# Optimization experiments

Measured on AMD Instinct MI355X. Metric: run time of the kernel, lower is better.

Reference implementation:

```python
import jax, jax.numpy as jnp
import numpy as np

NUM_RBF = 300
RADIUS_RES = 0.1
GAMMA = 10.0
HIDDEN = 64
MB, ATOM = 32, 64


def setup_inputs() -> dict:
    key = jax.random.key(0)
    ks = jax.random.split(key, 12)
    def lin(kw, kb, fan_in, fan_out):
        lim = 1.0 / np.sqrt(fan_in)
        W = jax.random.uniform(kw, (fan_out, fan_in), jnp.float32, -lim, lim)
        b = jax.random.uniform(kb, (fan_out,), jnp.float32, -lim, lim)
        return W, b
    W1, b1 = lin(ks[0], ks[1], HIDDEN, HIDDEN)
    W2, b2 = lin(ks[2], ks[3], HIDDEN, HIDDEN)
    W3, b3 = lin(ks[4], ks[5], HIDDEN, HIDDEN)
    Wd1, bd1 = lin(ks[6], ks[7], NUM_RBF, HIDDEN)
    Wd2, bd2 = lin(ks[8], ks[9], HIDDEN, HIDDEN)
    x = jax.random.normal(ks[10], (MB, ATOM, HIDDEN), jnp.float32)
    dist = jax.random.uniform(ks[11], (MB, ATOM, ATOM), jnp.float32, 0.0, 10.0)
    return {"x": x, "dist": dist,
            "W1": W1, "b1": b1, "W2": W2, "b2": b2, "W3": W3, "b3": b3,
            "Wd1": Wd1, "bd1": bd1, "Wd2": Wd2, "bd2": bd2}


def reference(x, dist, W1, b1, W2, b2, W3, b3, Wd1, bd1, Wd2, bd2):
    sp = jax.nn.softplus
    # linear1 applied per-atom
    v = jnp.einsum('mic,oc->mio', x, W1) + b1                      # [mb, atom, h]
    # CFConv: gaussian RBF expansion of pairwise distances
    centers = jnp.arange(NUM_RBF, dtype=jnp.float32) * RADIUS_RES  # [rbf]
    rbf = jnp.exp(-GAMMA * (dist[..., None] - centers) ** 2)       # [mb, a, a, rbf]
    # 2-layer filter MLP on each pair
    f = sp(jnp.einsum('mijr,hr->mijh', rbf, Wd1) + bd1)            # [mb, a, a, h]
    f = sp(jnp.einsum('mijh,oh->mijo', f, Wd2) + bd2)              # [mb, a, a, h]
    # broadcast-multiply v over pairs and reduce over source atom i (dim=1)
    v = jnp.einsum('mic,mijc->mjc', v, f)                          # [mb, atom, h]
    v = sp(jnp.einsum('mic,oc->mio', v, W2) + b2)
    v = jnp.einsum('mic,oc->mio', v, W3) + b3
    return x + v
```

## Files before the change

kernel.cpp:

```cpp
#include <hip/hip_runtime.h>
#include <math.h>

#define MB_    32
#define ATOM_  64
#define HID_   64
#define NRBF_  300
#define GAMMA_ 10.0f
#define RES_   0.1f

#define TPTS      2001
#define TSTEP     0.005f
#define INV_TSTEP 200.0f

#define RWIN 28

#define T_OFF   0
#define T_SZ    (TPTS * 64)
#define V1_OFF  (T_OFF + T_SZ)
#define V1_SZ   (MB_ * 64 * 64)
#define W2T_OFF (V1_OFF + V1_SZ)
#define W3T_OFF (W2T_OFF + 4096)

__device__ __forceinline__ float sp_f(float x) {
    return fmaxf(x, 0.f) + log1pf(__expf(-fabsf(x)));
}

__global__ __launch_bounds__(256)
void schnet_prep(const float* __restrict__ x,   const float* __restrict__ W1,
                 const float* __restrict__ b1,  const float* __restrict__ W2,
                 const float* __restrict__ W3,  const float* __restrict__ Wd1,
                 const float* __restrict__ bd1, const float* __restrict__ Wd2,
                 const float* __restrict__ bd2, float* __restrict__ ws)
{
    __shared__ float smem[8320];
    const int tid = threadIdx.x;
    const int b   = blockIdx.x;

    if (b < MB_) {
        float* sx = smem;
        float* sw = smem + 4160;
        const float* xm = x + b * 4096;
        for (int e = tid; e < 4096; e += 256) {
            int i = e >> 6, c = e & 63;
            sx[i * 65 + c] = xm[e];
            sw[i * 65 + c] = W1[e];
        }
        __syncthreads();
        const int tx = tid & 15;
        const int ty = tid >> 4;
        float acc[4][4];
        #pragma unroll
        for (int aa = 0; aa < 4; ++aa)
            #pragma unroll
            for (int bb = 0; bb < 4; ++bb)
                acc[aa][bb] = b1[4 * tx + bb];
        #pragma unroll 8
        for (int k = 0; k < 64; ++k) {
            float xa[4], wb[4];
            #pragma unroll
            for (int aa = 0; aa < 4; ++aa) xa[aa] = sx[(4 * ty + aa) * 65 + k];
            #pragma unroll
            for (int bb = 0; bb < 4; ++bb) wb[bb] = sw[(4 * tx + bb) * 65 + k];
            #pragma unroll
            for (int aa = 0; aa < 4; ++aa)
                #pragma unroll
                for (int bb = 0; bb < 4; ++bb)
                    acc[aa][bb] = fmaf(xa[aa], wb[bb], acc[aa][bb]);
        }
        #pragma unroll
        for (int aa = 0; aa < 4; ++aa) {
            float4 v = make_float4(acc[aa][0], acc[aa][1], acc[aa][2], acc[aa][3]);
            *(float4*)(ws + V1_OFF + (b * 64 + 4 * ty + aa) * 64 + 4 * tx) = v;
        }
    } else if (b < MB_ + 501) {
        float* su = smem;
        const int sub = tid >> 6, c = tid & 63;
        const int s  = (b - MB_) * 4 + sub;
        const int se = min(s, TPTS - 1);
        const float d = se * TSTEP;

        int r0 = (int)ceilf((d - 1.35f) * 10.0f);
        r0 = max(r0, 0);

        float a0 = bd1[c], a1 = 0.f;
        const float* wrow1 = Wd1 + c * NRBF_ + r0;
        #pragma unroll
        for (int k = 0; k < RWIN; k += 2) {
            float t0 = fmaf(-RES_, (float)(r0 + k),     d);
            float t1 = fmaf(-RES_, (float)(r0 + k + 1), d);
            float w0 = __expf(-GAMMA_ * t0 * t0);
            float w1 = __expf(-GAMMA_ * t1 * t1);
            a0 = fmaf(w0, wrow1[k],     a0);
            a1 = fmaf(w1, wrow1[k + 1], a1);
        }
        su[sub * 64 + c] = sp_f(a0 + a1);
        __syncthreads();

        const float4* wrow2 = (const float4*)(Wd2 + c * 64);
        const float*  uu    = su + sub * 64;
        float s0 = bd2[c], s1 = 0.f, s2 = 0.f, s3 = 0.f;
        #pragma unroll
        for (int h4 = 0; h4 < 16; ++h4) {
            float4 wv = wrow2[h4];
            s0 = fmaf(wv.x, uu[4 * h4 + 0], s0);
            s1 = fmaf(wv.y, uu[4 * h4 + 1], s1);
            s2 = fmaf(wv.z, uu[4 * h4 + 2], s2);
            s3 = fmaf(wv.w, uu[4 * h4 + 3], s3);
        }
        if (s < TPTS)
            ws[T_OFF + s * 64 + c] = sp_f((s0 + s1) + (s2 + s3));
    } else {
        for (int e = tid; e < 4096; e += 256) {
            int o = e >> 6, c = e & 63;
            ws[W2T_OFF + c * 64 + o] = W2[e];
            ws[W3T_OFF + c * 64 + o] = W3[e];
        }
    }
}

__global__ __launch_bounds__(256)
void schnet_main(const float* __restrict__ x, const float* __restrict__ dist,
                 const float* __restrict__ b2, const float* __restrict__ b3,
                 const float* __restrict__ ws, float* __restrict__ out)
{
    __shared__ float sD[64];
    __shared__ float sRed[4 * 64];
    const int m   = blockIdx.x >> 6;
    const int j   = blockIdx.x & 63;
    const int tid = threadIdx.x;
    const int c   = tid & 63;
    const int p   = tid >> 6;

    if (tid < 64) sD[tid] = dist[(m * ATOM_ + tid) * ATOM_ + j];
    __syncthreads();

    const float* Tb  = ws + T_OFF;
    const float* v1m = ws + V1_OFF + (m * 64 + p * 16) * 64;
    float acc = 0.f;
    #pragma unroll
    for (int ii = 0; ii < 16; ++ii) {
        float d  = sD[p * 16 + ii];
        float f  = d * INV_TSTEP;
        int   s  = min((int)f, TPTS - 2);
        float fr = f - (float)s;
        const float* Tr = Tb + s * 64;
        float t0 = Tr[c], t1 = Tr[64 + c];
        float f2v = fmaf(fr, t1 - t0, t0);
        acc = fmaf(f2v, v1m[ii * 64 + c], acc);
    }
    sRed[p * 64 + c] = acc;
    __syncthreads();
    if (tid < 64)
        sD[tid] = sRed[tid] + sRed[64 + tid] + sRed[128 + tid] + sRed[192 + tid];
    __syncthreads();

    {
        const float* W2t = ws + W2T_OFF;
        float s_ = 0.f;
        #pragma unroll
        for (int cc = 0; cc < 16; ++cc)
            s_ = fmaf(sD[16 * p + cc], W2t[(16 * p + cc) * 64 + c], s_);
        sRed[p * 64 + c] = s_;
    }
    __syncthreads();
    if (tid < 64)
        sD[tid] = sp_f(sRed[tid] + sRed[64 + tid] + sRed[128 + tid] + sRed[192 + tid] + b2[tid]);
    __syncthreads();
    {
        const float* W3t = ws + W3T_OFF;
        float s_ = 0.f;
        #pragma unroll
        for (int cc = 0; cc < 16; ++cc)
            s_ = fmaf(sD[16 * p + cc], W3t[(16 * p + cc) * 64 + c], s_);
        sRed[p * 64 + c] = s_;
    }
    __syncthreads();
    if (tid < 64) {
        float v_ = sRed[tid] + sRed[64 + tid] + sRed[128 + tid] + sRed[192 + tid] + b3[tid];
        out[(m * ATOM_ + j) * HID_ + tid] = v_ + x[(m * ATOM_ + j) * HID_ + tid];
    }
}

extern "C" void kernel_launch(void* const* d_in, const int* in_sizes, int n_in,
                              void* d_out, int out_size, void* d_ws, size_t ws_size,
                              hipStream_t stream) {
    const float* x   = (const float*)d_in[0];
    const float* dist= (const float*)d_in[1];
    const float* W1  = (const float*)d_in[2];
    const float* b1  = (const float*)d_in[3];
    const float* W2  = (const float*)d_in[4];
    const float* b2  = (const float*)d_in[5];
    const float* W3  = (const float*)d_in[6];
    const float* b3  = (const float*)d_in[7];
    const float* Wd1 = (const float*)d_in[8];
    const float* bd1 = (const float*)d_in[9];
    const float* Wd2 = (const float*)d_in[10];
    const float* bd2 = (const float*)d_in[11];
    float* out = (float*)d_out;
    float* ws  = (float*)d_ws;
    (void)in_sizes; (void)n_in; (void)out_size; (void)ws_size;

    schnet_prep<<<dim3(MB_ + 501 + 1), dim3(256), 0, stream>>>(
        x, W1, b1, W2, W3, Wd1, bd1, Wd2, bd2, ws);
    schnet_main<<<dim3(MB_ * ATOM_), dim3(256), 0, stream>>>(
        x, dist, b2, b3, ws, out);
}
```

Baseline: 92.88 us.

## Interleave lookup table pairs for float2 loads and stage filter weights in LDS

The filter lookup table now stores each sample's value next to the next sample's value, so the main kernel fetches both interpolation endpoints with a single float2 load instead of two scattered loads. This doubles the table's size and write traffic. In the prep kernel, each table-building block stages its Wd1 window and a transposed Wd2 in shared memory, replacing strided per-thread global reads with coalesced loads. The cost is extra shared memory use and an added barrier per block.

```diff
diff --git a/kernel.cpp b/kernel.cpp
--- a/kernel.cpp
+++ b/kernel.cpp
@@ -13,10 +13,11 @@
 #define INV_TSTEP 200.0f
 
 #define RWIN 28
-
-#define T_OFF   0
-#define T_SZ    (TPTS * 64)
-#define V1_OFF  (T_OFF + T_SZ)
+#define NSTG 32
+
+#define T2_OFF  0
+#define T2_SZ   (TPTS * 128)
+#define V1_OFF  (T2_OFF + T2_SZ)
 #define V1_SZ   (MB_ * 64 * 64)
 #define W2T_OFF (V1_OFF + V1_SZ)
 #define W3T_OFF (W2T_OFF + 4096)
@@ -41,9 +42,9 @@
         float* sw = smem + 4160;
         const float* xm = x + b * 4096;
         for (int e = tid; e < 4096; e += 256) {
-            int i = e >> 6, c = e & 63;
-            sx[i * 65 + c] = xm[e];
-            sw[i * 65 + c] = W1[e];
+            int i = e >> 6, cc = e & 63;
+            sx[i * 65 + cc] = xm[e];
+            sw[i * 65 + cc] = W1[e];
         }
         __syncthreads();
         const int tx = tid & 15;
@@ -73,47 +74,68 @@
             *(float4*)(ws + V1_OFF + (b * 64 + 4 * ty + aa) * 64 + 4 * tx) = v;
         }
     } else if (b < MB_ + 501) {
-        float* su = smem;
+        float* sWd1  = smem;
+        float* sWd2T = smem + NSTG * 65;
+        float* su    = smem + NSTG * 65 + 4160;
+
         const int sub = tid >> 6, c = tid & 63;
         const int s  = (b - MB_) * 4 + sub;
         const int se = min(s, TPTS - 1);
         const float d = se * TSTEP;
 
+        const int s0 = (b - MB_) * 4;
+        int rb0 = (int)ceilf((s0 * TSTEP - 1.35f) * 10.0f);
+        rb0 = max(rb0, 0);
         int r0 = (int)ceilf((d - 1.35f) * 10.0f);
         r0 = max(r0, 0);
 
+        #pragma unroll
+        for (int it = 0; it < (NSTG * 64) / 256; ++it) {
+            int idx = tid + it * 256;
+            int k   = idx & (NSTG - 1);
+            int cc  = idx >> 5;
+            sWd1[k * 65 + cc] = Wd1[cc * NRBF_ + rb0 + k];
+        }
+        #pragma unroll
+        for (int it = 0; it < 4096 / 256; ++it) {
+            int idx = tid + it * 256;
+            int h = idx & 63, o = idx >> 6;
+            sWd2T[h * 65 + o] = Wd2[idx];
+        }
+        __syncthreads();
+
         float a0 = bd1[c], a1 = 0.f;
-        const float* wrow1 = Wd1 + c * NRBF_ + r0;
+        const float* wr = sWd1 + (r0 - rb0) * 65 + c;
         #pragma unroll
         for (int k = 0; k < RWIN; k += 2) {
             float t0 = fmaf(-RES_, (float)(r0 + k),     d);
             float t1 = fmaf(-RES_, (float)(r0 + k + 1), d);
             float w0 = __expf(-GAMMA_ * t0 * t0);
             float w1 = __expf(-GAMMA_ * t1 * t1);
-            a0 = fmaf(w0, wrow1[k],     a0);
-            a1 = fmaf(w1, wrow1[k + 1], a1);
+            a0 = fmaf(w0, wr[k * 65],       a0);
+            a1 = fmaf(w1, wr[(k + 1) * 65], a1);
         }
         su[sub * 64 + c] = sp_f(a0 + a1);
         __syncthreads();
 
-        const float4* wrow2 = (const float4*)(Wd2 + c * 64);
-        const float*  uu    = su + sub * 64;
-        float s0 = bd2[c], s1 = 0.f, s2 = 0.f, s3 = 0.f;
-        #pragma unroll
-        for (int h4 = 0; h4 < 16; ++h4) {
-            float4 wv = wrow2[h4];
-            s0 = fmaf(wv.x, uu[4 * h4 + 0], s0);
-            s1 = fmaf(wv.y, uu[4 * h4 + 1], s1);
-            s2 = fmaf(wv.z, uu[4 * h4 + 2], s2);
-            s3 = fmaf(wv.w, uu[4 * h4 + 3], s3);
-        }
-        if (s < TPTS)
-            ws[T_OFF + s * 64 + c] = sp_f((s0 + s1) + (s2 + s3));
+        const float* uu = su + sub * 64;
+        float p0 = bd2[c], p1 = 0.f;
+        #pragma unroll
+        for (int h = 0; h < 64; h += 2) {
+            p0 = fmaf(sWd2T[h * 65 + c],       uu[h],     p0);
+            p1 = fmaf(sWd2T[(h + 1) * 65 + c], uu[h + 1], p1);
+        }
+        if (s < TPTS) {
+            float val = sp_f(p0 + p1);
+            float* T2 = ws + T2_OFF;
+            T2[s * 128 + 2 * c] = val;
+            if (s > 0) T2[(s - 1) * 128 + 2 * c + 1] = val;
+        }
     } else {
         for (int e = tid; e < 4096; e += 256) {
-            int o = e >> 6, c = e & 63;
-            ws[W2T_OFF + c * 64 + o] = W2[e];
-            ws[W3T_OFF + c * 64 + o] = W3[e];
+            int o = e >> 6, cc = e & 63;
+            ws[W2T_OFF + cc * 64 + o] = W2[e];
+            ws[W3T_OFF + cc * 64 + o] = W3[e];
         }
     }
 }
@@ -134,7 +156,7 @@
     if (tid < 64) sD[tid] = dist[(m * ATOM_ + tid) * ATOM_ + j];
     __syncthreads();
 
-    const float* Tb  = ws + T_OFF;
+    const float* Tb  = ws + T2_OFF;
     const float* v1m = ws + V1_OFF + (m * 64 + p * 16) * 64;
     float acc = 0.f;
     #pragma unroll
@@ -143,9 +165,8 @@
         float f  = d * INV_TSTEP;
         int   s  = min((int)f, TPTS - 2);
         float fr = f - (float)s;
-        const float* Tr = Tb + s * 64;
-        float t0 = Tr[c], t1 = Tr[64 + c];
-        float f2v = fmaf(fr, t1 - t0, t0);
+        float2 t = *(const float2*)(Tb + s * 128 + 2 * c);
+        float f2v = fmaf(fr, t.y - t.x, t.x);
         acc = fmaf(f2v, v1m[ii * 64 + c], acc);
     }
     sRed[p * 64 + c] = acc;
```

Result: no change. 93.10 us (+0.2%).
